# Performance work log

Measured on AMD Instinct MI355X. Metric: run time of the kernel, lower is better.

The kernel has to match this reference:

```python
import jax, jax.numpy as jnp
import numpy as np
from jax import lax

H = 1024          # Encoder_hidd == Decoder_hidd (fc consumes lstm1 output)
WIN_IN, WIN_OUT = 168, 24
B, F_IN = 256, 8
KEEP = 0.8        # 1 - dropout_probability(0.2)


def setup_inputs() -> dict:
    key = jax.random.key(0)
    ks = jax.random.split(key, 10)
    s = 1.0 / np.sqrt(H)
    return {
        "x":      jax.random.normal(ks[0], (B, WIN_IN + WIN_OUT, F_IN), jnp.float32),
        "conv_w": jax.random.normal(ks[1], (1, F_IN, 3), jnp.float32) * 0.2,  # [O,I,K]
        "conv_b": jnp.zeros((1,), jnp.float32),
        "Wih0":   jax.random.normal(ks[2], (4 * H, 1), jnp.float32) * s,
        "Whh0":   jax.random.normal(ks[3], (4 * H, H), jnp.float32) * s,
        "bih0":   jnp.zeros((4 * H,), jnp.float32),
        "bhh0":   jnp.zeros((4 * H,), jnp.float32),
        "Wih1":   jax.random.normal(ks[4], (4 * H, H), jnp.float32) * s,
        "Whh1":   jax.random.normal(ks[5], (4 * H, H), jnp.float32) * s,
        "bih1":   jnp.zeros((4 * H,), jnp.float32),
        "bhh1":   jnp.zeros((4 * H,), jnp.float32),
        "fc_w":   jax.random.normal(ks[6], (1, H), jnp.float32) * s,
        "fc_b":   jnp.zeros((1,), jnp.float32),
    }


def _forward(x, conv_w, conv_b, Wih0, Whh0, bih0, bhh0,
             Wih1, Whh1, bih1, bhh1, fc_w, fc_b):
    b0 = bih0 + bhh0
    b1 = bih1 + bhh1

    def cell(h0, c0, h1, c1, xt):
        # 2-layer LSTM cell, PyTorch gate order i, f, g, o
        g = xt @ Wih0.T + h0 @ Whh0.T + b0
        i, f, gg, o = jnp.split(g, 4, axis=-1)
        c0 = jax.nn.sigmoid(f) * c0 + jax.nn.sigmoid(i) * jnp.tanh(gg)
        h0 = jax.nn.sigmoid(o) * jnp.tanh(c0)
        g = h0 @ Wih1.T + h1 @ Whh1.T + b1
        i, f, gg, o = jnp.split(g, 4, axis=-1)
        c1 = jax.nn.sigmoid(f) * c1 + jax.nn.sigmoid(i) * jnp.tanh(gg)
        h1 = jax.nn.sigmoid(o) * jnp.tanh(c1)
        return h0, c0, h1, c1

    # ---- CNN front-end on encoder window ----
    xe = jnp.transpose(x[:, :WIN_IN, :], (0, 2, 1))            # [B, F_IN, 168]
    y = lax.conv_general_dilated(xe, conv_w, (1,), [(1, 1)],
                                 dimension_numbers=("NCH", "OIH", "NCH"))
    y = jax.nn.relu(y + conv_b[None, :, None])                 # [B, 1, 168]
    y = lax.reduce_window(y, -jnp.inf, lax.max,
                          (1, 1, 2), (1, 1, 2), "VALID")      # [B, 1, 84]
    seq = jnp.transpose(y, (2, 0, 1))                           # [84, B, 1]

    bsz = x.shape[0]
    z = jnp.zeros((bsz, H), x.dtype)

    def enc_step(carry, xt):
        return cell(*carry, xt), None

    carry, _ = lax.scan(enc_step, (z, z, z, z), seq)            # t=0 LSTM pass
    h1_last = carry[2]

    dkey = jax.random.key(42)

    def dropout(v, t):
        m = jax.random.bernoulli(jax.random.fold_in(dkey, t), KEEP, v.shape)
        return jnp.where(m, v / KEEP, jnp.zeros((), v.dtype))

    def fc(v):
        return v @ fc_w.T + fc_b

    y0 = fc(dropout(h1_last, 0))                                # [B, 1]

    def dec_step(carry, t):
        h0, c0, h1, c1, yp = carry
        h0, c0, h1, c1 = cell(h0, c0, h1, c1, yp)               # feed y_pred back
        yt = fc(dropout(h1, t))
        return (h0, c0, h1, c1, yt), yt

    _, ys = lax.scan(dec_step, (*carry, y0), jnp.arange(1, WIN_OUT))
    ys = jnp.swapaxes(ys, 0, 1)[..., 0]                         # [B, 23]
    return jnp.concatenate([y0, ys], axis=1)                    # [B, 24]


def reference(x, conv_w, conv_b, Wih0, Whh0, bih0, bhh0,
              Wih1, Whh1, bih1, bhh1, fc_w, fc_b):
    return _forward(x, conv_w, conv_b, Wih0, Whh0, bih0, bhh0,
                    Wih1, Whh1, bih1, bhh1, fc_w, fc_b)
```

## Files before the change

### kernel.cpp

```cpp
#include <hip/hip_runtime.h>
#include <stdint.h>

typedef _Float16 f16;
typedef f16  f16x8 __attribute__((ext_vector_type(8)));
typedef float f32x4 __attribute__((ext_vector_type(4)));
typedef unsigned u32x4 __attribute__((ext_vector_type(4)));

#define H0_OFF    0u
#define H1_OFF    2097152u
#define WHH0F_OFF 4194304u
#define SEQ_OFF   12582912u
#define YACC_OFF  12668928u
#define FLAG_OFF  12693504u

__device__ __forceinline__ unsigned rotl32(unsigned x, int d){ return (x<<d)|(x>>(32-d)); }

__device__ __forceinline__ uint2 tf2x32(unsigned k0, unsigned k1, unsigned x0, unsigned x1){
  unsigned kx = k0 ^ k1 ^ 0x1BD11BDAu;
  x0 += k0; x1 += k1;
#define TFR(r) { x0 += x1; x1 = rotl32(x1,(r)); x1 ^= x0; }
  TFR(13) TFR(15) TFR(26) TFR(6)  x0 += k1; x1 += kx + 1u;
  TFR(17) TFR(29) TFR(16) TFR(24) x0 += kx; x1 += k0 + 2u;
  TFR(13) TFR(15) TFR(26) TFR(6)  x0 += k0; x1 += k1 + 3u;
  TFR(17) TFR(29) TFR(16) TFR(24) x0 += k1; x1 += kx + 4u;
  TFR(13) TFR(15) TFR(26) TFR(6)  x0 += kx; x1 += k0 + 5u;
#undef TFR
  return make_uint2(x0, x1);
}

__device__ __forceinline__ bool drop_keep(uint2 fk, unsigned n){
  uint2 o = tf2x32(fk.x, fk.y, 0u, n);
  unsigned bits = o.x ^ o.y;
  float u = __uint_as_float((bits >> 9) | 0x3f800000u) - 1.0f;
  return u < 0.8f;
}

__device__ __forceinline__ float sigf(float x){ return 1.0f/(1.0f + __expf(-x)); }
__device__ __forceinline__ float thf(float x){ return 1.0f - 2.0f/(__expf(2.0f*x) + 1.0f); }

__device__ __forceinline__ void st_dword_sc(void* p, unsigned v){
  asm volatile("global_store_dword %0, %1, off sc0 sc1" :: "v"(p), "v"(v) : "memory");
}
__device__ __forceinline__ void st_dwordx4_sc(void* p, u32x4 v){
  asm volatile("global_store_dwordx4 %0, %1, off sc0 sc1" :: "v"(p), "v"(v) : "memory");
}
__device__ __forceinline__ unsigned ld_dword_sc(const void* p){
  unsigned r;
  asm volatile("global_load_dword %0, %1, off sc0 sc1\n\ts_waitcnt vmcnt(0)"
               : "=v"(r) : "v"(p) : "memory");
  return r;
}

__device__ __forceinline__ void gbar(unsigned* flagsH, unsigned* gflagsH, unsigned e,
                                     int tid, int lblk, bool inv){
  asm volatile("s_waitcnt vmcnt(0)" ::: "memory");
  __syncthreads();
  if (tid == 0) st_dword_sc(flagsH + lblk*32, e);
  if (lblk < 8){
    if (tid < 16){
      unsigned* f = flagsH + (lblk*16 + tid)*32;
      while (ld_dword_sc(f) < e) __builtin_amdgcn_s_sleep(1);
    }
    __syncthreads();
    if (tid == 0) st_dword_sc(gflagsH + lblk*32, e);
  }
  if (tid < 8){
    unsigned* f = gflagsH + tid*32;
    while (ld_dword_sc(f) < e) __builtin_amdgcn_s_sleep(1);
  }
  __syncthreads();
  if (inv) __builtin_amdgcn_fence(__ATOMIC_ACQUIRE, "agent");
  __builtin_amdgcn_sched_barrier(0);
}

__global__ void k_init(uint4* __restrict__ hz, uint4* __restrict__ yz, uint4* __restrict__ fz){
  unsigned i = blockIdx.x*256u + threadIdx.x;
  if (i < 262144u){ hz[i] = uint4{0,0,0,0}; }
  else if (i < 263680u){ yz[i - 262144u] = uint4{0,0,0,0}; }
  else if (i < 265856u){ fz[i - 263680u] = uint4{0,0,0,0}; }
}

__global__ void k_seq(const float* __restrict__ x, const float* __restrict__ cw,
                      const float* __restrict__ cb, float* __restrict__ seq){
  const int q = blockIdx.x;
  const int b = threadIdx.x;
  float best = -1e30f;
#pragma unroll
  for (int ssub = 0; ssub < 2; ++ssub){
    int p = 2*q + ssub;
    float acc = cb[0];
#pragma unroll
    for (int k = 0; k < 3; ++k){
      int t = p - 1 + k;
      if (t >= 0 && t < 168){
        const float* xp = x + ((size_t)b*192 + t)*8;
#pragma unroll
        for (int i = 0; i < 8; ++i) acc = fmaf(xp[i], cw[i*3 + k], acc);
      }
    }
    acc  = fmaxf(acc, 0.0f);
    best = fmaxf(best, acc);
  }
  seq[(q<<8) + b] = best;
}

__global__ void __launch_bounds__(512) k_wpack(const float* __restrict__ W, f16* __restrict__ dst){
  const int hgrp = blockIdx.x;
  const int tid = threadIdx.x;
  const int l   = tid & 63;
  const int w   = tid >> 6;
  const int j0  = hgrp << 3;
#pragma unroll
  for (int fi = 0; fi < 8; ++fi){
    const int f = (w << 3) + fi;
    const int c = f >> 1, T = f & 1;
    const int r = l & 15;
    const int u = (T << 2) + (r >> 2);
    const int g = r & 3;
    const float* src = W + (((size_t)((g << 10) + j0 + u)) << 10) + (c << 5) + ((l >> 4) << 3);
    float4 a = *(const float4*)src;
    float4 b = *(const float4*)(src + 4);
    f16x8 v;
    v[0]=(f16)a.x; v[1]=(f16)a.y; v[2]=(f16)a.z; v[3]=(f16)a.w;
    v[4]=(f16)b.x; v[5]=(f16)b.y; v[6]=(f16)b.z; v[7]=(f16)b.w;
    *(f16x8*)(dst + ((size_t)hgrp << 15) + (f << 9) + (l << 3)) = v;
  }
}

#define MFMA16(a,b,c) __builtin_amdgcn_mfma_f32_16x16x32_f16((a),(b),(c),0,0,0)

__global__ void __launch_bounds__(512, 1) k_main(
    const float* __restrict__ Wih0, const float* __restrict__ Whh0,
    const float* __restrict__ bih0, const float* __restrict__ bhh0,
    const float* __restrict__ Wih1, const float* __restrict__ Whh1,
    const float* __restrict__ bih1, const float* __restrict__ bhh1,
    const float* __restrict__ fc_w, const float* __restrict__ fc_b,
    char* __restrict__ ws, float* __restrict__ out)
{
  extern __shared__ char smem_[];
  f16* lds = (f16*)smem_;
  f16* stage  = lds + 65536;
  f16* wstage = lds + 66560;

  const int tid  = threadIdx.x;
  const int blk  = blockIdx.x;
  const int hgrp = blk & 127;
  const int bgrp = blk >> 7;
  const int j0   = hgrp << 3;
  const int l    = tid & 63;
  const int w8   = tid >> 6;
  const int q    = l >> 4;
  const int c16  = l & 15;
  const int lcol = (w8 << 4) + c16;
  const int bcol = (bgrp << 7) + lcol;

  {
    const float* srcs[2] = {Wih1, Whh1};
#pragma unroll
    for (int m = 0; m < 2; ++m){
#pragma unroll
      for (int fi = 0; fi < 8; ++fi){
        const int f = (w8 << 3) + fi;
        const int c = f >> 1, T = f & 1;
        const int r = c16;
        const int uu = (T << 2) + (r >> 2);
        const int g = r & 3;
        const float* src = srcs[m] + (((size_t)((g << 10) + j0 + uu)) << 10) + (c << 5) + (q << 3);
        float4 a = *(const float4*)src;
        float4 b = *(const float4*)(src + 4);
        f16x8 v;
        v[0]=(f16)a.x; v[1]=(f16)a.y; v[2]=(f16)a.z; v[3]=(f16)a.w;
        v[4]=(f16)b.x; v[5]=(f16)b.y; v[6]=(f16)b.z; v[7]=(f16)b.w;
        *(f16x8*)(lds + m*32768 + (f << 9) + (l << 3)) = v;
      }
    }
  }
  __syncthreads();

  float bias0t[2][4], bias1t[2][4], wi0t[2][4];
#pragma unroll
  for (int t = 0; t < 2; ++t){
    const int uu = j0 + q + t*4;
#pragma unroll
    for (int g = 0; g < 4; ++g){
      int row = (g << 10) + uu;
      bias0t[t][g] = bih0[row] + bhh0[row];
      bias1t[t][g] = bih1[row] + bhh1[row];
      wi0t[t][g]   = Wih0[row];
    }
  }
  const float fcw0 = fc_w[j0 + q] * 1.25f;
  const float fcw1 = fc_w[j0 + q + 4] * 1.25f;
  const float fcb  = fc_b[0];

  const int base_h = (q << 11) + (bcol << 3);

  f16* H0 = (f16*)(ws + H0_OFF);
  f16* H1 = (f16*)(ws + H1_OFF);
  const f16* whh0f = (const f16*)(ws + WHH0F_OFF) + ((size_t)hgrp << 15);
  const float* seq = (const float*)(ws + SEQ_OFF);
  float* y_acc = (float*)(ws + YACC_OFF);
  unsigned* flagsH  = (unsigned*)(ws + FLAG_OFF) + bgrp*4352;
  unsigned* gflagsH = flagsH + 128*32;

  u32x4 wreg[8];
#pragma unroll
  for (int ch = 0; ch < 8; ++ch)
    wreg[ch] = *(const u32x4*)(whh0f + ((size_t)ch << 12) + (tid << 3));

  f16x8 BhP[2][4];
  {
    const f16* a00 = H0 + base_h;
#pragma unroll
    for (int i = 0; i < 4; ++i){
      BhP[0][i] = *(const f16x8*)(a00 + i*8192);
      BhP[1][i] = *(const f16x8*)(a00 + (4+i)*8192);
    }
  }

  float c0[2] = {0,0}, c1[2] = {0,0};
  float yprev = 0.f;
  unsigned ep = 0;

#pragma unroll 1
  for (int s = 0; s < 107; ++s){
    const int src = s & 1, dst = src ^ 1;

    if (s >= 84){
      const int tp = s - 84;
      yprev = fcb + __uint_as_float(ld_dword_sc(y_acc + (tp << 8) + bcol));
      if (hgrp == 0 && q == 0) out[bcol*24 + tp] = yprev;
    }

    float h0n[2];
    {
      const f16* a0 = H0 + src*262144 + base_h;
      f32x4 acc0 = (f32x4){0,0,0,0}, acc1 = (f32x4){0,0,0,0};
      *(u32x4*)(wstage + (tid << 3)) = wreg[0];
      __syncthreads();
#define LDH(B, C0) { _Pragma("unroll") for (int i = 0; i < 4; ++i){ \
      BhP[B][i] = *(const f16x8*)(a0 + ((C0)+i)*8192); } }
#define MMW(B, CH) { const f16* wsb = wstage + (((CH)&1) << 12) + (l << 3); \
      _Pragma("unroll") for (int i = 0; i < 4; ++i){ \
      f16x8 wf0 = *(const f16x8*)(wsb + ((2*i  ) << 9)); \
      f16x8 wf1 = *(const f16x8*)(wsb + ((2*i+1) << 9)); \
      acc0 = MFMA16(wf0, BhP[B][i], acc0); \
      acc1 = MFMA16(wf1, BhP[B][i], acc1); } }
#pragma unroll
      for (int ch = 0; ch < 8; ++ch){
        if (ch < 7) *(u32x4*)(wstage + (((ch+1)&1) << 12) + (tid << 3)) = wreg[ch+1];
        MMW(ch&1, ch)
        if (ch < 6) LDH(ch&1, (ch+2)*4)
        if (ch < 7) __syncthreads();
      }
#undef LDH
#undef MMW
      float xb = (s < 84) ? seq[(s << 8) + bcol] : yprev;
      f32x4 at[2] = {acc0, acc1};
#pragma unroll
      for (int t = 0; t < 2; ++t){
        float pi = at[t][0] + bias0t[t][0] + wi0t[t][0]*xb;
        float pf = at[t][1] + bias0t[t][1] + wi0t[t][1]*xb;
        float pg = at[t][2] + bias0t[t][2] + wi0t[t][2]*xb;
        float po = at[t][3] + bias0t[t][3] + wi0t[t][3]*xb;
        c0[t]  = sigf(pf)*c0[t] + sigf(pi)*thf(pg);
        h0n[t] = sigf(po)*thf(c0[t]);
        stage[(lcol << 3) + q + t*4] = (f16)h0n[t];
      }
    }
    __syncthreads();
    if (tid < 128){
      u32x4 v = ((const u32x4*)stage)[tid];
      st_dwordx4_sc((char*)(H0 + dst*262144 + (hgrp << 11) + (bgrp << 10)) + tid*16, v);
    }
    ++ep; gbar(flagsH, gflagsH, ep, tid, hgrp, true);

    float h1n[2];
    {
      const f16* b0 = H0 + dst*262144 + base_h;
      const f16* b1 = H1 + src*262144 + base_h;
      f16x8 X0[2][4], X1[2][4];
      f32x4 acc0 = (f32x4){0,0,0,0}, acc1 = (f32x4){0,0,0,0};
#define LDB(B, CB) { _Pragma("unroll") for (int i = 0; i < 4; ++i){ const int c = (CB)+i; \
      X0[B][i] = *(const f16x8*)(b0 + c*8192); \
      X1[B][i] = *(const f16x8*)(b1 + c*8192); } }
#define MMB(B, CB) { _Pragma("unroll") for (int i = 0; i < 4; ++i){ const int c = (CB)+i; \
      f16x8 wa0 = *(const f16x8*)(lds + ((2*c  ) << 9) + (l << 3)); \
      f16x8 wa1 = *(const f16x8*)(lds + ((2*c+1) << 9) + (l << 3)); \
      f16x8 wb0 = *(const f16x8*)(lds + 32768 + ((2*c  ) << 9) + (l << 3)); \
      f16x8 wb1 = *(const f16x8*)(lds + 32768 + ((2*c+1) << 9) + (l << 3)); \
      acc0 = MFMA16(wa0, X0[B][i], acc0); \
      acc0 = MFMA16(wb0, X1[B][i], acc0); \
      acc1 = MFMA16(wa1, X0[B][i], acc1); \
      acc1 = MFMA16(wb1, X1[B][i], acc1); } }
      LDB(0, 0)
#pragma unroll
      for (int cb = 0; cb < 8; ++cb){
        if ((cb & 1) == 0){ if (cb < 7) LDB(1, (cb+1)*4) MMB(0, cb*4) }
        else              { if (cb < 7) LDB(0, (cb+1)*4) MMB(1, cb*4) }
      }
#undef LDB
#undef MMB
      f32x4 at[2] = {acc0, acc1};
#pragma unroll
      for (int t = 0; t < 2; ++t){
        float pi = at[t][0] + bias1t[t][0];
        float pf = at[t][1] + bias1t[t][1];
        float pg = at[t][2] + bias1t[t][2];
        float po = at[t][3] + bias1t[t][3];
        c1[t]  = sigf(pf)*c1[t] + sigf(pi)*thf(pg);
        h1n[t] = sigf(po)*thf(c1[t]);
        stage[(lcol << 3) + q + t*4] = (f16)h1n[t];
      }
    }
    __syncthreads();
    if (tid < 128){
      u32x4 v = ((const u32x4*)stage)[tid];
      st_dwordx4_sc((char*)(H1 + dst*262144 + (hgrp << 11) + (bgrp << 10)) + tid*16, v);
    }
    __syncthreads();

    {
      const f16* a0n = H0 + dst*262144 + base_h;
#pragma unroll
      for (int i = 0; i < 4; ++i){
        BhP[0][i] = *(const f16x8*)(a0n + i*8192);
        BhP[1][i] = *(const f16x8*)(a0n + (4+i)*8192);
      }
    }

    if (s >= 83){
      const int tau = s - 83;
      uint2 fk = tf2x32(0u, 42u, 0u, (unsigned)tau);
      unsigned n0 = ((unsigned)bcol << 10) + (unsigned)(j0 + q);
      unsigned n1 = n0 + 4u;
      float v = (drop_keep(fk, n0) ? h1n[0]*fcw0 : 0.f)
              + (drop_keep(fk, n1) ? h1n[1]*fcw1 : 0.f);
      v += __shfl_xor(v, 16, 64);
      v += __shfl_xor(v, 32, 64);
      if (q == 0) atomicAdd(y_acc + (tau << 8) + bcol, v);
      ++ep; gbar(flagsH, gflagsH, ep, tid, hgrp, false);
    }
  }

  if (hgrp == 0 && q == 0)
    out[bcol*24 + 23] = fcb + __uint_as_float(ld_dword_sc(y_acc + (23 << 8) + bcol));
}

extern "C" void kernel_launch(void* const* d_in, const int* in_sizes, int n_in,
                              void* d_out, int out_size, void* d_ws, size_t ws_size,
                              hipStream_t stream)
{
  const float* x    = (const float*)d_in[0];
  const float* cw   = (const float*)d_in[1];
  const float* cb   = (const float*)d_in[2];
  const float* Wih0 = (const float*)d_in[3];
  const float* Whh0 = (const float*)d_in[4];
  const float* bih0 = (const float*)d_in[5];
  const float* bhh0 = (const float*)d_in[6];
  const float* Wih1 = (const float*)d_in[7];
  const float* Whh1 = (const float*)d_in[8];
  const float* bih1 = (const float*)d_in[9];
  const float* bhh1 = (const float*)d_in[10];
  const float* fc_w = (const float*)d_in[11];
  const float* fc_b = (const float*)d_in[12];
  float* out = (float*)d_out;
  char*  ws  = (char*)d_ws;

  hipLaunchKernelGGL(k_init, dim3(1040), dim3(256), 0, stream,
                     (uint4*)(ws + H0_OFF), (uint4*)(ws + YACC_OFF), (uint4*)(ws + FLAG_OFF));
  hipLaunchKernelGGL(k_seq,  dim3(84), dim3(256), 0, stream, x, cw, cb, (float*)(ws + SEQ_OFF));
  hipLaunchKernelGGL(k_wpack, dim3(128), dim3(512), 0, stream, Whh0, (f16*)(ws + WHH0F_OFF));
  hipLaunchKernelGGL(k_main, dim3(256), dim3(512), 149504, stream,
                     Wih0, Whh0, bih0, bhh0, Wih1, Whh1, bih1, bhh1,
                     fc_w, fc_b, ws, out);
}
```

Measured before the change: 3.007 ms.

## Split hidden units across 512 persistent blocks with four units per block

The persistent LSTM kernel now gives each block 4 hidden units instead of 8 and launches 512 blocks instead of 256. Per-block LDS weight footprint and register weights are halved, and the grid barrier tree widens to 16 leaders. The goal is to spread the per-step GEMV work over more compute units and cut per-block latency on the serial recurrence. The cost is more barrier participants per step, smaller 8-byte publish stores, and reliance on all 512 blocks being co-resident (launch bounds now allow 4 per CU).

```diff
diff --git a/kernel.cpp b/kernel.cpp
--- a/kernel.cpp
+++ b/kernel.cpp
@@ -4,6 +4,7 @@
 typedef _Float16 f16;
 typedef f16  f16x8 __attribute__((ext_vector_type(8)));
 typedef float f32x4 __attribute__((ext_vector_type(4)));
+typedef unsigned u32x2 __attribute__((ext_vector_type(2)));
 typedef unsigned u32x4 __attribute__((ext_vector_type(4)));
 
 #define H0_OFF    0u
@@ -41,8 +42,8 @@
 __device__ __forceinline__ void st_dword_sc(void* p, unsigned v){
   asm volatile("global_store_dword %0, %1, off sc0 sc1" :: "v"(p), "v"(v) : "memory");
 }
-__device__ __forceinline__ void st_dwordx4_sc(void* p, u32x4 v){
-  asm volatile("global_store_dwordx4 %0, %1, off sc0 sc1" :: "v"(p), "v"(v) : "memory");
+__device__ __forceinline__ void st_dwordx2_sc(void* p, u32x2 v){
+  asm volatile("global_store_dwordx2 %0, %1, off sc0 sc1" :: "v"(p), "v"(v) : "memory");
 }
 __device__ __forceinline__ unsigned ld_dword_sc(const void* p){
   unsigned r;
@@ -56,7 +57,7 @@
   asm volatile("s_waitcnt vmcnt(0)" ::: "memory");
   __syncthreads();
   if (tid == 0) st_dword_sc(flagsH + lblk*32, e);
-  if (lblk < 8){
+  if (lblk < 16){
     if (tid < 16){
       unsigned* f = flagsH + (lblk*16 + tid)*32;
       while (ld_dword_sc(f) < e) __builtin_amdgcn_s_sleep(1);
@@ -64,7 +65,7 @@
     __syncthreads();
     if (tid == 0) st_dword_sc(gflagsH + lblk*32, e);
   }
-  if (tid < 8){
+  if (tid < 16){
     unsigned* f = gflagsH + tid*32;
     while (ld_dword_sc(f) < e) __builtin_amdgcn_s_sleep(1);
   }
@@ -77,7 +78,7 @@
   unsigned i = blockIdx.x*256u + threadIdx.x;
   if (i < 262144u){ hz[i] = uint4{0,0,0,0}; }
   else if (i < 263680u){ yz[i - 262144u] = uint4{0,0,0,0}; }
-  else if (i < 265856u){ fz[i - 263680u] = uint4{0,0,0,0}; }
+  else if (i < 268032u){ fz[i - 263680u] = uint4{0,0,0,0}; }
 }
 
 __global__ void k_seq(const float* __restrict__ x, const float* __restrict__ cw,
@@ -109,27 +110,26 @@
   const int tid = threadIdx.x;
   const int l   = tid & 63;
   const int w   = tid >> 6;
-  const int j0  = hgrp << 3;
-#pragma unroll
-  for (int fi = 0; fi < 8; ++fi){
-    const int f = (w << 3) + fi;
-    const int c = f >> 1, T = f & 1;
+  const int j0  = hgrp << 2;
+#pragma unroll
+  for (int fi = 0; fi < 4; ++fi){
+    const int f = (w << 2) + fi;
     const int r = l & 15;
-    const int u = (T << 2) + (r >> 2);
+    const int u = r >> 2;
     const int g = r & 3;
-    const float* src = W + (((size_t)((g << 10) + j0 + u)) << 10) + (c << 5) + ((l >> 4) << 3);
+    const float* src = W + (((size_t)((g << 10) + j0 + u)) << 10) + (f << 5) + ((l >> 4) << 3);
     float4 a = *(const float4*)src;
     float4 b = *(const float4*)(src + 4);
     f16x8 v;
     v[0]=(f16)a.x; v[1]=(f16)a.y; v[2]=(f16)a.z; v[3]=(f16)a.w;
     v[4]=(f16)b.x; v[5]=(f16)b.y; v[6]=(f16)b.z; v[7]=(f16)b.w;
-    *(f16x8*)(dst + ((size_t)hgrp << 15) + (f << 9) + (l << 3)) = v;
+    *(f16x8*)(dst + ((size_t)hgrp << 14) + (f << 9) + (l << 3)) = v;
   }
 }
 
 #define MFMA16(a,b,c) __builtin_amdgcn_mfma_f32_16x16x32_f16((a),(b),(c),0,0,0)
 
-__global__ void __launch_bounds__(512, 1) k_main(
+__global__ void __launch_bounds__(512, 4) k_main(
     const float* __restrict__ Wih0, const float* __restrict__ Whh0,
     const float* __restrict__ bih0, const float* __restrict__ bhh0,
     const float* __restrict__ Wih1, const float* __restrict__ Whh1,
@@ -138,15 +138,15 @@
     char* __restrict__ ws, float* __restrict__ out)
 {
   extern __shared__ char smem_[];
-  f16* lds = (f16*)smem_;
-  f16* stage  = lds + 65536;
-  f16* wstage = lds + 66560;
+  f16* lds    = (f16*)smem_;
+  f16* stage  = lds + 32768;
+  f16* wstage = lds + 33280;
 
   const int tid  = threadIdx.x;
   const int blk  = blockIdx.x;
-  const int hgrp = blk & 127;
-  const int bgrp = blk >> 7;
-  const int j0   = hgrp << 3;
+  const int hgrp = blk & 255;
+  const int bgrp = blk >> 8;
+  const int j0   = hgrp << 2;
   const int l    = tid & 63;
   const int w8   = tid >> 6;
   const int q    = l >> 4;
@@ -159,54 +159,50 @@
 #pragma unroll
     for (int m = 0; m < 2; ++m){
 #pragma unroll
-      for (int fi = 0; fi < 8; ++fi){
-        const int f = (w8 << 3) + fi;
-        const int c = f >> 1, T = f & 1;
+      for (int fi = 0; fi < 4; ++fi){
+        const int f = (w8 << 2) + fi;
         const int r = c16;
-        const int uu = (T << 2) + (r >> 2);
+        const int uu = r >> 2;
         const int g = r & 3;
-        const float* src = srcs[m] + (((size_t)((g << 10) + j0 + uu)) << 10) + (c << 5) + (q << 3);
+        const float* src = srcs[m] + (((size_t)((g << 10) + j0 + uu)) << 10) + (f << 5) + (q << 3);
         float4 a = *(const float4*)src;
         float4 b = *(const float4*)(src + 4);
         f16x8 v;
         v[0]=(f16)a.x; v[1]=(f16)a.y; v[2]=(f16)a.z; v[3]=(f16)a.w;
         v[4]=(f16)b.x; v[5]=(f16)b.y; v[6]=(f16)b.z; v[7]=(f16)b.w;
-        *(f16x8*)(lds + m*32768 + (f << 9) + (l << 3)) = v;
+        *(f16x8*)(lds + m*16384 + (f << 9) + (l << 3)) = v;
       }
     }
   }
   __syncthreads();
 
-  float bias0t[2][4], bias1t[2][4], wi0t[2][4];
-#pragma unroll
-  for (int t = 0; t < 2; ++t){
-    const int uu = j0 + q + t*4;
-#pragma unroll
-    for (int g = 0; g < 4; ++g){
-      int row = (g << 10) + uu;
-      bias0t[t][g] = bih0[row] + bhh0[row];
-      bias1t[t][g] = bih1[row] + bhh1[row];
-      wi0t[t][g]   = Wih0[row];
-    }
-  }
-  const float fcw0 = fc_w[j0 + q] * 1.25f;
-  const float fcw1 = fc_w[j0 + q + 4] * 1.25f;
+  float bias0g[4], bias1g[4], wi0g[4];
+#pragma unroll
+  for (int g = 0; g < 4; ++g){
+    int row = (g << 10) + j0 + q;
+    bias0g[g] = bih0[row] + bhh0[row];
+    bias1g[g] = bih1[row] + bhh1[row];
+    wi0g[g]   = Wih0[row];
+  }
+  const float fcwq = fc_w[j0 + q] * 1.25f;
   const float fcb  = fc_b[0];
 
   const int base_h = (q << 11) + (bcol << 3);
 
   f16* H0 = (f16*)(ws + H0_OFF);
   f16* H1 = (f16*)(ws + H1_OFF);
-  const f16* whh0f = (const f16*)(ws + WHH0F_OFF) + ((size_t)hgrp << 15);
+  const f16* whh0f = (const f16*)(ws + WHH0F_OFF) + ((size_t)hgrp << 14);
   const float* seq = (const float*)(ws + SEQ_OFF);
   float* y_acc = (float*)(ws + YACC_OFF);
-  unsigned* flagsH  = (unsigned*)(ws + FLAG_OFF) + bgrp*4352;
-  unsigned* gflagsH = flagsH + 128*32;
-
-  u32x4 wreg[8];
+  unsigned* flagsH  = (unsigned*)(ws + FLAG_OFF) + bgrp*8704;
+  unsigned* gflagsH = flagsH + 256*32;
+
+  const int puboff = ((hgrp >> 1) << 11) + ((hgrp & 1) << 2);
+
+  u32x2 wreg[8];
 #pragma unroll
   for (int ch = 0; ch < 8; ++ch)
-    wreg[ch] = *(const u32x4*)(whh0f + ((size_t)ch << 12) + (tid << 3));
+    wreg[ch] = *(const u32x2*)(whh0f + (ch << 11) + (tid << 2));
 
   f16x8 BhP[2][4];
   {
@@ -218,8 +214,7 @@
     }
   }
 
-  float c0[2] = {0,0}, c1[2] = {0,0};
-  float yprev = 0.f;
+  float c0 = 0.f, c1 = 0.f, yprev = 0.f;
   unsigned ep = 0;
 
 #pragma unroll 1
@@ -232,23 +227,21 @@
       if (hgrp == 0 && q == 0) out[bcol*24 + tp] = yprev;
     }
 
-    float h0n[2];
+    float h0n;
     {
       const f16* a0 = H0 + src*262144 + base_h;
-      f32x4 acc0 = (f32x4){0,0,0,0}, acc1 = (f32x4){0,0,0,0};
-      *(u32x4*)(wstage + (tid << 3)) = wreg[0];
+      f32x4 acc = (f32x4){0,0,0,0};
+      *(u32x2*)(wstage + (tid << 2)) = wreg[0];
       __syncthreads();
 #define LDH(B, C0) { _Pragma("unroll") for (int i = 0; i < 4; ++i){ \
       BhP[B][i] = *(const f16x8*)(a0 + ((C0)+i)*8192); } }
-#define MMW(B, CH) { const f16* wsb = wstage + (((CH)&1) << 12) + (l << 3); \
+#define MMW(B, CH) { const f16* wsb = wstage + (((CH)&1) << 11) + (l << 3); \
       _Pragma("unroll") for (int i = 0; i < 4; ++i){ \
-      f16x8 wf0 = *(const f16x8*)(wsb + ((2*i  ) << 9)); \
-      f16x8 wf1 = *(const f16x8*)(wsb + ((2*i+1) << 9)); \
-      acc0 = MFMA16(wf0, BhP[B][i], acc0); \
-      acc1 = MFMA16(wf1, BhP[B][i], acc1); } }
+      f16x8 wf = *(const f16x8*)(wsb + (i << 9)); \
+      acc = MFMA16(wf, BhP[B][i], acc); } }
 #pragma unroll
       for (int ch = 0; ch < 8; ++ch){
-        if (ch < 7) *(u32x4*)(wstage + (((ch+1)&1) << 12) + (tid << 3)) = wreg[ch+1];
+        if (ch < 7) *(u32x2*)(wstage + (((ch+1)&1) << 11) + (tid << 2)) = wreg[ch+1];
         MMW(ch&1, ch)
         if (ch < 6) LDH(ch&1, (ch+2)*4)
         if (ch < 7) __syncthreads();
@@ -256,43 +249,35 @@
 #undef LDH
 #undef MMW
       float xb = (s < 84) ? seq[(s << 8) + bcol] : yprev;
-      f32x4 at[2] = {acc0, acc1};
-#pragma unroll
-      for (int t = 0; t < 2; ++t){
-        float pi = at[t][0] + bias0t[t][0] + wi0t[t][0]*xb;
-        float pf = at[t][1] + bias0t[t][1] + wi0t[t][1]*xb;
-        float pg = at[t][2] + bias0t[t][2] + wi0t[t][2]*xb;
-        float po = at[t][3] + bias0t[t][3] + wi0t[t][3]*xb;
-        c0[t]  = sigf(pf)*c0[t] + sigf(pi)*thf(pg);
-        h0n[t] = sigf(po)*thf(c0[t]);
-        stage[(lcol << 3) + q + t*4] = (f16)h0n[t];
-      }
+      float pi = acc[0] + bias0g[0] + wi0g[0]*xb;
+      float pf = acc[1] + bias0g[1] + wi0g[1]*xb;
+      float pg = acc[2] + bias0g[2] + wi0g[2]*xb;
+      float po = acc[3] + bias0g[3] + wi0g[3]*xb;
+      c0  = sigf(pf)*c0 + sigf(pi)*thf(pg);
+      h0n = sigf(po)*thf(c0);
+      stage[(lcol << 2) + q] = (f16)h0n;
     }
     __syncthreads();
     if (tid < 128){
-      u32x4 v = ((const u32x4*)stage)[tid];
-      st_dwordx4_sc((char*)(H0 + dst*262144 + (hgrp << 11) + (bgrp << 10)) + tid*16, v);
+      u32x2 v = ((const u32x2*)stage)[tid];
+      st_dwordx2_sc((char*)(H0 + dst*262144 + puboff + (((bgrp << 7) + tid) << 3)) , v);
     }
     ++ep; gbar(flagsH, gflagsH, ep, tid, hgrp, true);
 
-    float h1n[2];
+    float h1n;
     {
       const f16* b0 = H0 + dst*262144 + base_h;
       const f16* b1 = H1 + src*262144 + base_h;
       f16x8 X0[2][4], X1[2][4];
-      f32x4 acc0 = (f32x4){0,0,0,0}, acc1 = (f32x4){0,0,0,0};
+      f32x4 acc = (f32x4){0,0,0,0};
 #define LDB(B, CB) { _Pragma("unroll") for (int i = 0; i < 4; ++i){ const int c = (CB)+i; \
       X0[B][i] = *(const f16x8*)(b0 + c*8192); \
       X1[B][i] = *(const f16x8*)(b1 + c*8192); } }
 #define MMB(B, CB) { _Pragma("unroll") for (int i = 0; i < 4; ++i){ const int c = (CB)+i; \
-      f16x8 wa0 = *(const f16x8*)(lds + ((2*c  ) << 9) + (l << 3)); \
-      f16x8 wa1 = *(const f16x8*)(lds + ((2*c+1) << 9) + (l << 3)); \
-      f16x8 wb0 = *(const f16x8*)(lds + 32768 + ((2*c  ) << 9) + (l << 3)); \
-      f16x8 wb1 = *(const f16x8*)(lds + 32768 + ((2*c+1) << 9) + (l << 3)); \
-      acc0 = MFMA16(wa0, X0[B][i], acc0); \
-      acc0 = MFMA16(wb0, X1[B][i], acc0); \
-      acc1 = MFMA16(wa1, X0[B][i], acc1); \
-      acc1 = MFMA16(wb1, X1[B][i], acc1); } }
+      f16x8 wa = *(const f16x8*)(lds + (c << 9) + (l << 3)); \
+      f16x8 wb = *(const f16x8*)(lds + 16384 + (c << 9) + (l << 3)); \
+      acc = MFMA16(wa, X0[B][i], acc); \
+      acc = MFMA16(wb, X1[B][i], acc); } }
       LDB(0, 0)
 #pragma unroll
       for (int cb = 0; cb < 8; ++cb){
@@ -301,22 +286,18 @@
       }
 #undef LDB
 #undef MMB
-      f32x4 at[2] = {acc0, acc1};
-#pragma unroll
-      for (int t = 0; t < 2; ++t){
-        float pi = at[t][0] + bias1t[t][0];
-        float pf = at[t][1] + bias1t[t][1];
-        float pg = at[t][2] + bias1t[t][2];
-        float po = at[t][3] + bias1t[t][3];
-        c1[t]  = sigf(pf)*c1[t] + sigf(pi)*thf(pg);
-        h1n[t] = sigf(po)*thf(c1[t]);
-        stage[(lcol << 3) + q + t*4] = (f16)h1n[t];
-      }
+      float pi = acc[0] + bias1g[0];
+      float pf = acc[1] + bias1g[1];
+      float pg = acc[2] + bias1g[2];
+      float po = acc[3] + bias1g[3];
+      c1  = sigf(pf)*c1 + sigf(pi)*thf(pg);
+      h1n = sigf(po)*thf(c1);
+      stage[(lcol << 2) + q] = (f16)h1n;
     }
     __syncthreads();
     if (tid < 128){
-      u32x4 v = ((const u32x4*)stage)[tid];
-      st_dwordx4_sc((char*)(H1 + dst*262144 + (hgrp << 11) + (bgrp << 10)) + tid*16, v);
+      u32x2 v = ((const u32x2*)stage)[tid];
+      st_dwordx2_sc((char*)(H1 + dst*262144 + puboff + (((bgrp << 7) + tid) << 3)) , v);
     }
     __syncthreads();
 
@@ -332,10 +313,8 @@
     if (s >= 83){
       const int tau = s - 83;
       uint2 fk = tf2x32(0u, 42u, 0u, (unsigned)tau);
-      unsigned n0 = ((unsigned)bcol << 10) + (unsigned)(j0 + q);
-      unsigned n1 = n0 + 4u;
-      float v = (drop_keep(fk, n0) ? h1n[0]*fcw0 : 0.f)
-              + (drop_keep(fk, n1) ? h1n[1]*fcw1 : 0.f);
+      unsigned n = ((unsigned)bcol << 10) + (unsigned)(j0 + q);
+      float v = drop_keep(fk, n) ? h1n*fcwq : 0.f;
       v += __shfl_xor(v, 16, 64);
       v += __shfl_xor(v, 32, 64);
       if (q == 0) atomicAdd(y_acc + (tau << 8) + bcol, v);
@@ -367,11 +346,11 @@
   float* out = (float*)d_out;
   char*  ws  = (char*)d_ws;
 
-  hipLaunchKernelGGL(k_init, dim3(1040), dim3(256), 0, stream,
+  hipLaunchKernelGGL(k_init, dim3(1047), dim3(256), 0, stream,
                      (uint4*)(ws + H0_OFF), (uint4*)(ws + YACC_OFF), (uint4*)(ws + FLAG_OFF));
   hipLaunchKernelGGL(k_seq,  dim3(84), dim3(256), 0, stream, x, cw, cb, (float*)(ws + SEQ_OFF));
-  hipLaunchKernelGGL(k_wpack, dim3(128), dim3(512), 0, stream, Whh0, (f16*)(ws + WHH0F_OFF));
-  hipLaunchKernelGGL(k_main, dim3(256), dim3(512), 149504, stream,
+  hipLaunchKernelGGL(k_wpack, dim3(256), dim3(512), 0, stream, Whh0, (f16*)(ws + WHH0F_OFF));
+  hipLaunchKernelGGL(k_main, dim3(512), dim3(512), 74752, stream,
                      Wih0, Whh0, bih0, bhh0, Wih1, Whh1, bih1, bhh1,
                      fc_w, fc_b, ws, out);
 }
```

Result: slower. 5.680 ms (+88.9%).

## Skew LSTM layers so layer-0 step t+1 shares a matmul pass with layer-1 step t

Applied to the files above, without the earlier changes.

Restructures the recurrent loop so the layer-0 recurrent matmul for the next timestep and the layer-1 matmul for the current timestep are computed in one fused pass. Both read the same freshly written h0 loads, so the separate H0 reload and one weight-staging sweep per step are folded together. Layer 0 is peeled for the first step, and its gate update runs after the layer-1 update. The aim is to cut per-step loads and barriers on the serial critical path, at the cost of more complex indexing for buffer parity and grid-barrier ordering.

```diff
diff --git a/kernel.cpp b/kernel.cpp
--- a/kernel.cpp
+++ b/kernel.cpp
@@ -208,100 +208,75 @@
   for (int ch = 0; ch < 8; ++ch)
     wreg[ch] = *(const u32x4*)(whh0f + ((size_t)ch << 12) + (tid << 3));
 
-  f16x8 BhP[2][4];
+  float c0[2] = {0,0}, c1[2] = {0,0};
+  unsigned ep = 0;
+
   {
-    const f16* a00 = H0 + base_h;
-#pragma unroll
-    for (int i = 0; i < 4; ++i){
-      BhP[0][i] = *(const f16x8*)(a00 + i*8192);
-      BhP[1][i] = *(const f16x8*)(a00 + (4+i)*8192);
-    }
-  }
-
-  float c0[2] = {0,0}, c1[2] = {0,0};
-  float yprev = 0.f;
-  unsigned ep = 0;
+    float xb = seq[bcol];
+#pragma unroll
+    for (int t = 0; t < 2; ++t){
+      float pi = bias0t[t][0] + wi0t[t][0]*xb;
+      float pf = bias0t[t][1] + wi0t[t][1]*xb;
+      float pg = bias0t[t][2] + wi0t[t][2]*xb;
+      float po = bias0t[t][3] + wi0t[t][3]*xb;
+      c0[t] = sigf(pi)*thf(pg);
+      float h0n = sigf(po)*thf(c0[t]);
+      stage[(lcol << 3) + q + t*4] = (f16)h0n;
+    }
+  }
+  __syncthreads();
+  if (tid < 128){
+    u32x4 v = ((const u32x4*)stage)[tid];
+    st_dwordx4_sc((char*)(H0 + 262144 + (hgrp << 11) + (bgrp << 10)) + tid*16, v);
+  }
+  ++ep; gbar(flagsH, gflagsH, ep, tid, hgrp, true);
 
 #pragma unroll 1
   for (int s = 0; s < 107; ++s){
-    const int src = s & 1, dst = src ^ 1;
-
-    if (s >= 84){
-      const int tp = s - 84;
-      yprev = fcb + __uint_as_float(ld_dword_sc(y_acc + (tp << 8) + bcol));
-      if (hgrp == 0 && q == 0) out[bcol*24 + tp] = yprev;
-    }
-
-    float h0n[2];
-    {
-      const f16* a0 = H0 + src*262144 + base_h;
-      f32x4 acc0 = (f32x4){0,0,0,0}, acc1 = (f32x4){0,0,0,0};
-      *(u32x4*)(wstage + (tid << 3)) = wreg[0];
-      __syncthreads();
-#define LDH(B, C0) { _Pragma("unroll") for (int i = 0; i < 4; ++i){ \
-      BhP[B][i] = *(const f16x8*)(a0 + ((C0)+i)*8192); } }
+    const int p = s & 1;
+    const bool doA = (s < 106);
+    const f16* hb0 = H0 + (p^1)*262144 + base_h;
+    const f16* hb1 = H1 + p*262144 + base_h;
+
+    f16x8 X0[2][4], X1[2][4];
+    f32x4 accB0 = (f32x4){0,0,0,0}, accB1 = (f32x4){0,0,0,0};
+    f32x4 accA0 = (f32x4){0,0,0,0}, accA1 = (f32x4){0,0,0,0};
+#define LDX(B, CB) { _Pragma("unroll") for (int i = 0; i < 4; ++i){ const int c = (CB)+i; \
+      X0[B][i] = *(const f16x8*)(hb0 + c*8192); \
+      X1[B][i] = *(const f16x8*)(hb1 + c*8192); } }
 #define MMW(B, CH) { const f16* wsb = wstage + (((CH)&1) << 12) + (l << 3); \
       _Pragma("unroll") for (int i = 0; i < 4; ++i){ \
       f16x8 wf0 = *(const f16x8*)(wsb + ((2*i  ) << 9)); \
       f16x8 wf1 = *(const f16x8*)(wsb + ((2*i+1) << 9)); \
-      acc0 = MFMA16(wf0, BhP[B][i], acc0); \
-      acc1 = MFMA16(wf1, BhP[B][i], acc1); } }
-#pragma unroll
-      for (int ch = 0; ch < 8; ++ch){
-        if (ch < 7) *(u32x4*)(wstage + (((ch+1)&1) << 12) + (tid << 3)) = wreg[ch+1];
-        MMW(ch&1, ch)
-        if (ch < 6) LDH(ch&1, (ch+2)*4)
-        if (ch < 7) __syncthreads();
-      }
-#undef LDH
-#undef MMW
-      float xb = (s < 84) ? seq[(s << 8) + bcol] : yprev;
-      f32x4 at[2] = {acc0, acc1};
-#pragma unroll
-      for (int t = 0; t < 2; ++t){
-        float pi = at[t][0] + bias0t[t][0] + wi0t[t][0]*xb;
-        float pf = at[t][1] + bias0t[t][1] + wi0t[t][1]*xb;
-        float pg = at[t][2] + bias0t[t][2] + wi0t[t][2]*xb;
-        float po = at[t][3] + bias0t[t][3] + wi0t[t][3]*xb;
-        c0[t]  = sigf(pf)*c0[t] + sigf(pi)*thf(pg);
-        h0n[t] = sigf(po)*thf(c0[t]);
-        stage[(lcol << 3) + q + t*4] = (f16)h0n[t];
-      }
-    }
-    __syncthreads();
-    if (tid < 128){
-      u32x4 v = ((const u32x4*)stage)[tid];
-      st_dwordx4_sc((char*)(H0 + dst*262144 + (hgrp << 11) + (bgrp << 10)) + tid*16, v);
-    }
-    ++ep; gbar(flagsH, gflagsH, ep, tid, hgrp, true);
-
-    float h1n[2];
-    {
-      const f16* b0 = H0 + dst*262144 + base_h;
-      const f16* b1 = H1 + src*262144 + base_h;
-      f16x8 X0[2][4], X1[2][4];
-      f32x4 acc0 = (f32x4){0,0,0,0}, acc1 = (f32x4){0,0,0,0};
-#define LDB(B, CB) { _Pragma("unroll") for (int i = 0; i < 4; ++i){ const int c = (CB)+i; \
-      X0[B][i] = *(const f16x8*)(b0 + c*8192); \
-      X1[B][i] = *(const f16x8*)(b1 + c*8192); } }
+      accA0 = MFMA16(wf0, X0[B][i], accA0); \
+      accA1 = MFMA16(wf1, X0[B][i], accA1); } }
 #define MMB(B, CB) { _Pragma("unroll") for (int i = 0; i < 4; ++i){ const int c = (CB)+i; \
       f16x8 wa0 = *(const f16x8*)(lds + ((2*c  ) << 9) + (l << 3)); \
       f16x8 wa1 = *(const f16x8*)(lds + ((2*c+1) << 9) + (l << 3)); \
       f16x8 wb0 = *(const f16x8*)(lds + 32768 + ((2*c  ) << 9) + (l << 3)); \
       f16x8 wb1 = *(const f16x8*)(lds + 32768 + ((2*c+1) << 9) + (l << 3)); \
-      acc0 = MFMA16(wa0, X0[B][i], acc0); \
-      acc0 = MFMA16(wb0, X1[B][i], acc0); \
-      acc1 = MFMA16(wa1, X0[B][i], acc1); \
-      acc1 = MFMA16(wb1, X1[B][i], acc1); } }
-      LDB(0, 0)
-#pragma unroll
-      for (int cb = 0; cb < 8; ++cb){
-        if ((cb & 1) == 0){ if (cb < 7) LDB(1, (cb+1)*4) MMB(0, cb*4) }
-        else              { if (cb < 7) LDB(0, (cb+1)*4) MMB(1, cb*4) }
-      }
-#undef LDB
+      accB0 = MFMA16(wa0, X0[B][i], accB0); \
+      accB0 = MFMA16(wb0, X1[B][i], accB0); \
+      accB1 = MFMA16(wa1, X0[B][i], accB1); \
+      accB1 = MFMA16(wb1, X1[B][i], accB1); } }
+    LDX(0, 0) LDX(1, 4)
+    *(u32x4*)(wstage + (tid << 3)) = wreg[0];
+    __syncthreads();
+#pragma unroll
+    for (int ch = 0; ch < 8; ++ch){
+      if (ch < 7) *(u32x4*)(wstage + (((ch+1)&1) << 12) + (tid << 3)) = wreg[ch+1];
+      if (doA) MMW(ch&1, ch)
+      MMB(ch&1, ch*4)
+      if (ch < 6) LDX(ch&1, (ch+2)*4)
+      if (ch < 7) __syncthreads();
+    }
+#undef LDX
+#undef MMW
 #undef MMB
-      f32x4 at[2] = {acc0, acc1};
+
+    float h1n[2];
+    {
+      f32x4 at[2] = {accB0, accB1};
 #pragma unroll
       for (int t = 0; t < 2; ++t){
         float pi = at[t][0] + bias1t[t][0];
@@ -316,17 +291,7 @@
     __syncthreads();
     if (tid < 128){
       u32x4 v = ((const u32x4*)stage)[tid];
-      st_dwordx4_sc((char*)(H1 + dst*262144 + (hgrp << 11) + (bgrp << 10)) + tid*16, v);
-    }
-    __syncthreads();
-
-    {
-      const f16* a0n = H0 + dst*262144 + base_h;
-#pragma unroll
-      for (int i = 0; i < 4; ++i){
-        BhP[0][i] = *(const f16x8*)(a0n + i*8192);
-        BhP[1][i] = *(const f16x8*)(a0n + (4+i)*8192);
-      }
+      st_dwordx4_sc((char*)(H1 + (p^1)*262144 + (hgrp << 11) + (bgrp << 10)) + tid*16, v);
     }
 
     if (s >= 83){
@@ -340,6 +305,38 @@
       v += __shfl_xor(v, 32, 64);
       if (q == 0) atomicAdd(y_acc + (tau << 8) + bcol, v);
       ++ep; gbar(flagsH, gflagsH, ep, tid, hgrp, false);
+    } else {
+      __syncthreads();
+    }
+
+    if (doA){
+      const int s1 = s + 1;
+      float xb;
+      if (s1 < 84){
+        xb = seq[(s1 << 8) + bcol];
+      } else {
+        const int tp = s1 - 84;
+        float yp = fcb + __uint_as_float(ld_dword_sc(y_acc + (tp << 8) + bcol));
+        if (hgrp == 0 && q == 0) out[bcol*24 + tp] = yp;
+        xb = yp;
+      }
+      f32x4 at[2] = {accA0, accA1};
+#pragma unroll
+      for (int t = 0; t < 2; ++t){
+        float pi = at[t][0] + bias0t[t][0] + wi0t[t][0]*xb;
+        float pf = at[t][1] + bias0t[t][1] + wi0t[t][1]*xb;
+        float pg = at[t][2] + bias0t[t][2] + wi0t[t][2]*xb;
+        float po = at[t][3] + bias0t[t][3] + wi0t[t][3]*xb;
+        c0[t]  = sigf(pf)*c0[t] + sigf(pi)*thf(pg);
+        float h0n = sigf(po)*thf(c0[t]);
+        stage[(lcol << 3) + q + t*4] = (f16)h0n;
+      }
+      __syncthreads();
+      if (tid < 128){
+        u32x4 v = ((const u32x4*)stage)[tid];
+        st_dwordx4_sc((char*)(H0 + p*262144 + (hgrp << 11) + (bgrp << 10)) + tid*16, v);
+      }
+      ++ep; gbar(flagsH, gflagsH, ep, tid, hgrp, true);
     }
   }
 
```

After: 2.865 ms. -4.7%, faster.
